# Performance work log

Hardware: AMD Instinct MI355X
Metric: run time of the kernel (lower is better)

Reference implementation:

```python
import jax, jax.numpy as jnp
import numpy as np

N = 4096        # nodes
D = 512         # in_dim = hidden_dim
E = 131072      # edges (avg degree 32)
K = 3           # aggregate_range
ALPHA = 2.0


def prelu(x, a):
    return jnp.where(x >= 0, x, a * x)


def setup_inputs() -> dict:
    key = jax.random.key(0)
    ks = jax.random.split(key, 8)
    s = 1.0 / np.sqrt(D)  # ~xavier scale
    return {
        "coeffs": jax.random.normal(ks[0], (N, D), jnp.float32),
        "edge_index": jax.random.randint(ks[1], (2, E), 0, N, dtype=jnp.int32),
        "W0": jax.random.normal(ks[2], (D, D), jnp.float32) * s,
        "b0": jnp.zeros((D,), jnp.float32),
        "a0": jnp.full((1,), 0.25, jnp.float32),
        "W1": jax.random.normal(ks[3], (D, D), jnp.float32) * s,  # use_bias=False
        "a1": jnp.full((1,), 0.25, jnp.float32),
        "W2": jax.random.normal(ks[4], (D, D), jnp.float32) * s,
        "a2": jnp.full((1,), 0.25, jnp.float32),
        "Wo": jax.random.normal(ks[5], (1, D), jnp.float32) * s,
        "bo": jnp.zeros((1,), jnp.float32),
    }


def _mlp(coeffs, W0, b0, a0, W1, a1, W2, a2, Wo, bo):
    # Linear+PReLU, then n_hidden_layers x [Linear(no bias)+PReLU+(Dropout: eval, no-op)], then Linear
    x = prelu(coeffs @ W0.T + b0, a0)
    x = prelu(x @ W1.T, a1)
    x = prelu(x @ W2.T, a2)
    return x @ Wo.T + bo  # [N, 1]


def _aggregate_k_hop(edge_index, angles):
    # Faithful to the torch code: enhanced_angles aliases angles, so each hop
    # reads the CURRENT (already enhanced) values:  a <- a + w_k * A_k @ a.
    # Hop 1 uses raw edge list (duplicate edges add twice). Hops >= 2 use
    # np.unique-deduplicated composed paths == boolean adjacency powers.
    src, dst = edge_index[0], edge_index[1]
    a = angles
    a = a + (0.5 ** ALPHA) * jax.ops.segment_sum(a[dst], src, num_segments=N)
    A = jnp.zeros((N, N), jnp.float32).at[src, dst].set(1.0)  # dedup'd boolean adjacency
    Ak = A
    for k_ in range(K - 1):
        Ak = ((Ak @ A) > 0).astype(jnp.float32)  # unique k-hop paths
        a = a + (1.0 / (k_ + 3)) ** ALPHA * (Ak @ a)
    return a


def reference(coeffs, edge_index, W0, b0, a0, W1, a1, W2, a2, Wo, bo):
    angles = _mlp(coeffs, W0, b0, a0, W1, a1, W2, a2, Wo, bo)
    return _aggregate_k_hop(edge_index, angles)
```

## Files before the change

### kernel.cpp

```cpp
#include <hip/hip_runtime.h>

#define N_NODES 4096
#define D_DIM   512
#define E_EDGES 131072
#define NWORDS  128

typedef __bf16 bf16;
typedef __bf16 bf16x4 __attribute__((ext_vector_type(4)));
typedef __bf16 bf16x8 __attribute__((ext_vector_type(8)));
typedef float  f32x4  __attribute__((ext_vector_type(4)));
typedef unsigned int u32;

#define GLOAD_LDS16(gp, lp) \
    __builtin_amdgcn_global_load_lds((const __attribute__((address_space(1))) u32*)(gp), \
                                     (__attribute__((address_space(3))) u32*)(lp), 16, 0, 0)

static const size_t OFF_W1B = 0;
static const size_t OFF_W2B = OFF_W1B + (size_t)D_DIM*D_DIM*2;
static const size_t OFF_X1  = OFF_W2B + (size_t)D_DIM*D_DIM*2;
static const size_t OFF_X2  = OFF_X1  + (size_t)N_NODES*D_DIM*2;
static const size_t OFF_ANG = OFF_X2  + (size_t)N_NODES*D_DIM*2;
static const size_t OFF_H1  = OFF_ANG + N_NODES*4;
static const size_t OFF_A2V = OFF_H1  + N_NODES*4;
static const size_t OFF_TP  = OFF_A2V + N_NODES*4;
static const size_t OFF_AB  = OFF_TP  + 1024*4;
static const size_t OFF_A2B = OFF_AB  + (size_t)N_NODES*NWORDS*4;
static const size_t OFF_A3B = OFF_A2B + (size_t)N_NODES*NWORDS*4;

__device__ __forceinline__ bf16x8 cvt8(float4 lo, float4 hi) {
    bf16x8 r;
    r[0] = (bf16)lo.x; r[1] = (bf16)lo.y; r[2] = (bf16)lo.z; r[3] = (bf16)lo.w;
    r[4] = (bf16)hi.x; r[5] = (bf16)hi.y; r[6] = (bf16)hi.z; r[7] = (bf16)hi.w;
    return r;
}

template<int MODE>
__global__ __launch_bounds__(256)
void gemm_fused(const float* __restrict__ Xf, const float* __restrict__ Wf,
                const bf16* __restrict__ X, const bf16* __restrict__ W,
                bf16* __restrict__ outB,
                const float* __restrict__ bias, const float* __restrict__ slope,
                const float* __restrict__ Wo, float* __restrict__ ang,
                const float* __restrict__ bo, float* __restrict__ h1,
                const float* __restrict__ W1f, const float* __restrict__ W2f,
                bf16* __restrict__ W1b, bf16* __restrict__ W2b,
                const int* __restrict__ esrc, const int* __restrict__ edst,
                u32* __restrict__ AbOut,
                const u32* __restrict__ P, const u32* __restrict__ Q, u32* __restrict__ BOut)
{
    __shared__ bf16 At[2][64][64];
    __shared__ bf16 Bt[2][64][64];
    __shared__ int  s_cnt[4];
    __shared__ int  s_list[4][256];
    const int bx = blockIdx.x;
    const int t = threadIdx.x;
    const int wave = t >> 6, lane = t & 63;

    if (bx < 512) {
        const int wm = wave >> 1, wn = wave & 1;
        const int quad = lane >> 4, lq = lane & 15;
        const int rowBase = (bx >> 3) * 64;
        const int colBase = (bx & 7) * 64;
        const int c0 = t, c1 = t + 256;
        const int r0 = c0 >> 3, o0 = (c0 & 7) * 8;
        const int r1 = c1 >> 3, o1 = (c1 & 7) * 8;

        f32x4 acc[2][2] = {};
        int cur = 0;

        if (MODE == 0) {
            const float* gA0 = Xf + (size_t)(rowBase + r0) * D_DIM + o0;
            const float* gA1 = Xf + (size_t)(rowBase + r1) * D_DIM + o1;
            const float* gB0 = Wf + (size_t)(colBase + r0) * D_DIM + o0;
            const float* gB1 = Wf + (size_t)(colBase + r1) * D_DIM + o1;
            float4 pa0l = *(const float4*)(gA0),     pa0h = *(const float4*)(gA0 + 4);
            float4 pa1l = *(const float4*)(gA1),     pa1h = *(const float4*)(gA1 + 4);
            float4 pb0l = *(const float4*)(gB0),     pb0h = *(const float4*)(gB0 + 4);
            float4 pb1l = *(const float4*)(gB1),     pb1h = *(const float4*)(gB1 + 4);
            for (int k0 = 0; k0 < D_DIM; k0 += 64) {
                *(bf16x8*)&At[cur][r0][o0] = cvt8(pa0l, pa0h);
                *(bf16x8*)&At[cur][r1][o1] = cvt8(pa1l, pa1h);
                *(bf16x8*)&Bt[cur][r0][o0] = cvt8(pb0l, pb0h);
                *(bf16x8*)&Bt[cur][r1][o1] = cvt8(pb1l, pb1h);
                if (k0 + 64 < D_DIM) {
                    pa0l = *(const float4*)(gA0 + k0 + 64); pa0h = *(const float4*)(gA0 + k0 + 68);
                    pa1l = *(const float4*)(gA1 + k0 + 64); pa1h = *(const float4*)(gA1 + k0 + 68);
                    pb0l = *(const float4*)(gB0 + k0 + 64); pb0h = *(const float4*)(gB0 + k0 + 68);
                    pb1l = *(const float4*)(gB1 + k0 + 64); pb1h = *(const float4*)(gB1 + k0 + 68);
                }
                __syncthreads();
                #pragma unroll
                for (int kc = 0; kc < 2; ++kc) {
                    bf16x8 af[2], bfr[2];
                    #pragma unroll
                    for (int tm = 0; tm < 2; ++tm) af[tm]  = *(const bf16x8*)&At[cur][wm * 32 + tm * 16 + lq][kc * 32 + quad * 8];
                    #pragma unroll
                    for (int tn = 0; tn < 2; ++tn) bfr[tn] = *(const bf16x8*)&Bt[cur][wn * 32 + tn * 16 + lq][kc * 32 + quad * 8];
                    #pragma unroll
                    for (int tm = 0; tm < 2; ++tm)
                        #pragma unroll
                        for (int tn = 0; tn < 2; ++tn)
                            acc[tm][tn] = __builtin_amdgcn_mfma_f32_16x16x32_bf16(af[tm], bfr[tn], acc[tm][tn], 0, 0, 0);
                }
                cur ^= 1;
            }
        } else {
            const bf16* gA0 = X + (size_t)(rowBase + r0) * D_DIM + o0;
            const bf16* gA1 = X + (size_t)(rowBase + r1) * D_DIM + o1;
            const bf16* gB0 = W + (size_t)(colBase + r0) * D_DIM + o0;
            const bf16* gB1 = W + (size_t)(colBase + r1) * D_DIM + o1;
            char* baseA = (char*)&At[0][0][0];
            char* baseB = (char*)&Bt[0][0][0];
            GLOAD_LDS16(gA0, baseA + wave * 1024);
            GLOAD_LDS16(gA1, baseA + 4096 + wave * 1024);
            GLOAD_LDS16(gB0, baseB + wave * 1024);
            GLOAD_LDS16(gB1, baseB + 4096 + wave * 1024);
            for (int k0 = 0; k0 < D_DIM; k0 += 64) {
                __syncthreads();
                if (k0 + 64 < D_DIM) {
                    int nb = (cur ^ 1) * 8192;
                    GLOAD_LDS16(gA0 + k0 + 64, baseA + nb + wave * 1024);
                    GLOAD_LDS16(gA1 + k0 + 64, baseA + nb + 4096 + wave * 1024);
                    GLOAD_LDS16(gB0 + k0 + 64, baseB + nb + wave * 1024);
                    GLOAD_LDS16(gB1 + k0 + 64, baseB + nb + 4096 + wave * 1024);
                }
                #pragma unroll
                for (int kc = 0; kc < 2; ++kc) {
                    bf16x8 af[2], bfr[2];
                    #pragma unroll
                    for (int tm = 0; tm < 2; ++tm) af[tm]  = *(const bf16x8*)&At[cur][wm * 32 + tm * 16 + lq][kc * 32 + quad * 8];
                    #pragma unroll
                    for (int tn = 0; tn < 2; ++tn) bfr[tn] = *(const bf16x8*)&Bt[cur][wn * 32 + tn * 16 + lq][kc * 32 + quad * 8];
                    #pragma unroll
                    for (int tm = 0; tm < 2; ++tm)
                        #pragma unroll
                        for (int tn = 0; tn < 2; ++tn)
                            acc[tm][tn] = __builtin_amdgcn_mfma_f32_16x16x32_bf16(af[tm], bfr[tn], acc[tm][tn], 0, 0, 0);
                }
                cur ^= 1;
            }
        }

        const float a = slope[0];
        if (MODE == 2) {
            float wo[2];
            #pragma unroll
            for (int tn = 0; tn < 2; ++tn) wo[tn] = Wo[colBase + wn * 32 + tn * 16 + lq];
            #pragma unroll
            for (int tm = 0; tm < 2; ++tm) {
                #pragma unroll
                for (int r = 0; r < 4; ++r) {
                    float p = 0.f;
                    #pragma unroll
                    for (int tn = 0; tn < 2; ++tn) {
                        float v = acc[tm][tn][r];
                        v = (v >= 0.f) ? v : a * v;
                        p += v * wo[tn];
                    }
                    #pragma unroll
                    for (int m = 1; m < 16; m <<= 1) p += __shfl_xor(p, m, 64);
                    if (lq == 0)
                        atomicAdd(&ang[rowBase + wm * 32 + tm * 16 + quad * 4 + r], p);
                }
            }
        } else {
            #pragma unroll
            for (int tm = 0; tm < 2; ++tm) {
                #pragma unroll
                for (int tn = 0; tn < 2; ++tn) {
                    int col = colBase + wn * 32 + tn * 16 + lq;
                    float b = (MODE == 0) ? bias[col] : 0.f;
                    #pragma unroll
                    for (int r = 0; r < 4; ++r) {
                        int row = rowBase + wm * 32 + tm * 16 + quad * 4 + r;
                        float v = acc[tm][tn][r] + b;
                        v = (v >= 0.f) ? v : a * v;
                        outB[(size_t)row * D_DIM + col] = (bf16)v;
                    }
                }
            }
        }
    } else if (MODE == 0) {
        if (bx < 640) {
            int base = (bx - 512) * 256 + t;
            for (int e = base; e < E_EDGES; e += 128 * 256) {
                int r = esrc[e], c = edst[e];
                atomicOr(&AbOut[(size_t)r * NWORDS + (c >> 5)], 1u << (c & 31));
            }
        } else if (bx < 768) {
            int cb = bx - 640;
            const float* src = (cb < 64) ? W1f : W2f;
            bf16* dst = (cb < 64) ? W1b : W2b;
            size_t base = (size_t)(cb & 63) * 4096;
            #pragma unroll
            for (int i = 0; i < 4; ++i) {
                size_t e = base + (size_t)(i * 256 + t) * 4;
                float4 v = *(const float4*)(src + e);
                bf16x4 o; o.x = (bf16)v.x; o.y = (bf16)v.y; o.z = (bf16)v.z; o.w = (bf16)v.w;
                *(bf16x4*)(dst + e) = o;
            }
        } else {
            float b = bo[0];
            for (int i = t; i < N_NODES; i += 256) { ang[i] = b; h1[i] = 0.f; }
        }
    } else {
        int row = (bx - 512) * 4 + wave;
        if (lane == 0) s_cnt[wave] = 0;
        __syncthreads();
        const u32* prow = P + (size_t)row * NWORDS;
        #pragma unroll
        for (int h = 0; h < 2; ++h) {
            u32 bits = prow[h * 64 + lane];
            int base = (h * 64 + lane) * 32;
            while (bits) {
                int b = __ffs(bits) - 1; bits &= bits - 1;
                int pos = atomicAdd(&s_cnt[wave], 1);
                if (pos < 256) s_list[wave][pos] = base + b;
            }
        }
        __syncthreads();
        int cnt = min(s_cnt[wave], 256);
        u32 acc0 = 0, acc1 = 0;
        int j = 0;
        for (; j + 4 <= cnt; j += 4) {
            int i0 = s_list[wave][j], i1 = s_list[wave][j + 1];
            int i2 = s_list[wave][j + 2], i3 = s_list[wave][j + 3];
            const u32* q0 = Q + (size_t)i0 * NWORDS;
            const u32* q1 = Q + (size_t)i1 * NWORDS;
            const u32* q2 = Q + (size_t)i2 * NWORDS;
            const u32* q3 = Q + (size_t)i3 * NWORDS;
            u32 x0 = q0[lane], x1 = q1[lane], x2 = q2[lane], x3 = q3[lane];
            u32 y0 = q0[64 + lane], y1 = q1[64 + lane], y2 = q2[64 + lane], y3 = q3[64 + lane];
            acc0 |= x0 | x1 | x2 | x3;
            acc1 |= y0 | y1 | y2 | y3;
        }
        for (; j < cnt; ++j) {
            const u32* q = Q + (size_t)s_list[wave][j] * NWORDS;
            acc0 |= q[lane]; acc1 |= q[64 + lane];
        }
        BOut[(size_t)row * NWORDS + lane]      = acc0;
        BOut[(size_t)row * NWORDS + 64 + lane] = acc1;
    }
}

__global__ __launch_bounds__(256)
void hop1_edges(const int* __restrict__ src, const int* __restrict__ dst,
                const float* __restrict__ ang, float* __restrict__ h1)
{
    int e = blockIdx.x * 256 + threadIdx.x;
    if (e < E_EDGES) atomicAdd(&h1[src[e]], 0.25f * ang[dst[e]]);
}

__global__ __launch_bounds__(256)
void bits_matvec2(const u32* __restrict__ A2, const float* __restrict__ ang,
                  const float* __restrict__ h1, float* __restrict__ a2,
                  float* __restrict__ Tpart)
{
    __shared__ float s_red[4];
    int wave = threadIdx.x >> 6, lane = threadIdx.x & 63;
    int row  = blockIdx.x * 4 + wave;
    float s = 0.f;
    #pragma unroll
    for (int h = 0; h < 2; ++h) {
        u32 bits = A2[(size_t)row * NWORDS + h * 64 + lane];
        int base = (h * 64 + lane) * 32;
        while (bits) {
            int b = __ffs(bits) - 1;
            bits &= bits - 1;
            s += ang[base + b] + h1[base + b];
        }
    }
    #pragma unroll
    for (int off = 32; off > 0; off >>= 1) s += __shfl_down(s, off, 64);
    if (lane == 0) {
        float val = (ang[row] + h1[row]) + (1.f / 9.f) * s;
        a2[row] = val;
        s_red[wave] = val;
    }
    __syncthreads();
    if (threadIdx.x == 0)
        Tpart[blockIdx.x] = s_red[0] + s_red[1] + s_red[2] + s_red[3];
}

__global__ __launch_bounds__(256)
void bits_matvec3(const u32* __restrict__ A3, const float* __restrict__ a2,
                  const float* __restrict__ Tpart, float* __restrict__ out)
{
    __shared__ float s_part[4];
    int wave = threadIdx.x >> 6, lane = threadIdx.x & 63;

    float tsum = 0.f;
    #pragma unroll
    for (int i = 0; i < 4; ++i) tsum += Tpart[i * 256 + threadIdx.x];
    #pragma unroll
    for (int off = 32; off > 0; off >>= 1) tsum += __shfl_down(tsum, off, 64);
    if (lane == 0) s_part[wave] = tsum;
    __syncthreads();
    const float T = s_part[0] + s_part[1] + s_part[2] + s_part[3];

    int row = blockIdx.x * 4 + wave;
    float s = 0.f;
    #pragma unroll
    for (int h = 0; h < 2; ++h) {
        u32 bits = ~A3[(size_t)row * NWORDS + h * 64 + lane];
        int base = (h * 64 + lane) * 32;
        while (bits) {
            int b = __ffs(bits) - 1;
            bits &= bits - 1;
            s += a2[base + b];
        }
    }
    #pragma unroll
    for (int off = 32; off > 0; off >>= 1) s += __shfl_down(s, off, 64);
    if (lane == 0) out[row] = a2[row] + (1.f / 16.f) * (T - s);
}

extern "C" void kernel_launch(void* const* d_in, const int* in_sizes, int n_in,
                              void* d_out, int out_size, void* d_ws, size_t ws_size,
                              hipStream_t stream) {
    const float* coeffs = (const float*)d_in[0];
    const int*   edges  = (const int*)d_in[1];
    const float* W0     = (const float*)d_in[2];
    const float* b0     = (const float*)d_in[3];
    const float* pa0    = (const float*)d_in[4];
    const float* W1     = (const float*)d_in[5];
    const float* pa1    = (const float*)d_in[6];
    const float* W2     = (const float*)d_in[7];
    const float* pa2    = (const float*)d_in[8];
    const float* Wo     = (const float*)d_in[9];
    const float* bo     = (const float*)d_in[10];
    float* out = (float*)d_out;

    char* ws = (char*)d_ws;
    bf16*  W1b  = (bf16*)(ws + OFF_W1B);
    bf16*  W2b  = (bf16*)(ws + OFF_W2B);
    bf16*  x1b  = (bf16*)(ws + OFF_X1);
    bf16*  x2b  = (bf16*)(ws + OFF_X2);
    float* ang  = (float*)(ws + OFF_ANG);
    float* h1   = (float*)(ws + OFF_H1);
    float* a2v  = (float*)(ws + OFF_A2V);
    float* Tp   = (float*)(ws + OFF_TP);
    u32*   Ab   = (u32*)(ws + OFF_AB);
    u32*   A2b  = (u32*)(ws + OFF_A2B);
    u32*   A3b  = (u32*)(ws + OFF_A3B);

    const int* srcp = edges;
    const int* dstp = edges + E_EDGES;

    hipMemsetAsync(Ab, 0, (size_t)N_NODES * NWORDS * 4, stream);

    gemm_fused<0><<<769, 256, 0, stream>>>(coeffs, W0, nullptr, nullptr, x1b, b0, pa0,
                                           nullptr, ang, bo, h1, W1, W2, W1b, W2b,
                                           srcp, dstp, Ab, nullptr, nullptr, nullptr);
    gemm_fused<1><<<1536, 256, 0, stream>>>(nullptr, nullptr, x1b, W1b, x2b, nullptr, pa1,
                                            nullptr, nullptr, nullptr, nullptr, nullptr, nullptr,
                                            nullptr, nullptr, nullptr, nullptr, nullptr, Ab, Ab, A2b);
    gemm_fused<2><<<1536, 256, 0, stream>>>(nullptr, nullptr, x2b, W2b, nullptr, nullptr, pa2,
                                            Wo, ang, nullptr, nullptr, nullptr, nullptr, nullptr, nullptr,
                                            nullptr, nullptr, nullptr, Ab, A2b, A3b);

    hop1_edges<<<E_EDGES / 256, 256, 0, stream>>>(srcp, dstp, ang, h1);
    bits_matvec2<<<N_NODES / 4, 256, 0, stream>>>(A2b, ang, h1, a2v, Tp);
    bits_matvec3<<<N_NODES / 4, 256, 0, stream>>>(A3b, a2v, Tp, out);
}
```

Measured before the change: 146.3 us.

## Fuse hop1, matvec2 and matvec3 into one persistent kernel with grid barriers

```diff
diff --git a/kernel.cpp b/kernel.cpp
--- a/kernel.cpp
+++ b/kernel.cpp
@@ -4,6 +4,7 @@
 #define D_DIM   512
 #define E_EDGES 131072
 #define NWORDS  128
+#define FIN_BLOCKS 512
 
 typedef __bf16 bf16;
 typedef __bf16 bf16x4 __attribute__((ext_vector_type(4)));
@@ -202,6 +203,7 @@
         } else {
             float b = bo[0];
             for (int i = t; i < N_NODES; i += 256) { ang[i] = b; h1[i] = 0.f; }
+            if (t < 4) BOut[t] = 0u;
         }
     } else {
         int row = (bx - 512) * 4 + wave;
@@ -244,75 +246,88 @@
 }
 
 __global__ __launch_bounds__(256)
-void hop1_edges(const int* __restrict__ src, const int* __restrict__ dst,
-                const float* __restrict__ ang, float* __restrict__ h1)
+void finalize(const int* __restrict__ src, const int* __restrict__ dst,
+              const float* __restrict__ ang, float* __restrict__ h1,
+              const u32* __restrict__ A2, float* __restrict__ a2,
+              const u32* __restrict__ A3, float* __restrict__ out,
+              int* __restrict__ bar, float* __restrict__ Tacc)
 {
-    int e = blockIdx.x * 256 + threadIdx.x;
-    if (e < E_EDGES) atomicAdd(&h1[src[e]], 0.25f * ang[dst[e]]);
-}
-
-__global__ __launch_bounds__(256)
-void bits_matvec2(const u32* __restrict__ A2, const float* __restrict__ ang,
-                  const float* __restrict__ h1, float* __restrict__ a2,
-                  float* __restrict__ Tpart)
-{
-    __shared__ float s_red[4];
-    int wave = threadIdx.x >> 6, lane = threadIdx.x & 63;
-    int row  = blockIdx.x * 4 + wave;
-    float s = 0.f;
+    __shared__ float s_red[8];
+    __shared__ float s_T;
+    const int t = threadIdx.x, wave = t >> 6, lane = t & 63;
+    const int bx = blockIdx.x;
+
+    {
+        int e = bx * 256 + t;
+        atomicAdd(&h1[src[e]], 0.25f * ang[dst[e]]);
+    }
+
+    __threadfence();
+    __syncthreads();
+    if (t == 0) {
+        __hip_atomic_fetch_add(bar, 1, __ATOMIC_ACQ_REL, __HIP_MEMORY_SCOPE_AGENT);
+        while (__hip_atomic_load(bar, __ATOMIC_ACQUIRE, __HIP_MEMORY_SCOPE_AGENT) < FIN_BLOCKS) {}
+    }
+    __syncthreads();
+    __threadfence();
+
     #pragma unroll
-    for (int h = 0; h < 2; ++h) {
-        u32 bits = A2[(size_t)row * NWORDS + h * 64 + lane];
-        int base = (h * 64 + lane) * 32;
-        while (bits) {
-            int b = __ffs(bits) - 1;
-            bits &= bits - 1;
-            s += ang[base + b] + h1[base + b];
-        }
-    }
+    for (int rr = 0; rr < 2; ++rr) {
+        int row = bx * 8 + wave * 2 + rr;
+        float s = 0.f;
+        #pragma unroll
+        for (int h = 0; h < 2; ++h) {
+            u32 bits = A2[(size_t)row * NWORDS + h * 64 + lane];
+            int base = (h * 64 + lane) * 32;
+            while (bits) {
+                int b = __ffs(bits) - 1; bits &= bits - 1;
+                s += ang[base + b] + h1[base + b];
+            }
+        }
+        #pragma unroll
+        for (int off = 32; off > 0; off >>= 1) s += __shfl_down(s, off, 64);
+        if (lane == 0) {
+            float val = (ang[row] + h1[row]) + (1.f / 9.f) * s;
+            a2[row] = val;
+            s_red[wave * 2 + rr] = val;
+        }
+    }
+    __syncthreads();
+    if (t == 0) {
+        float p = 0.f;
+        #pragma unroll
+        for (int i = 0; i < 8; ++i) p += s_red[i];
+        __hip_atomic_fetch_add(Tacc, p, __ATOMIC_RELAXED, __HIP_MEMORY_SCOPE_AGENT);
+    }
+
+    __threadfence();
+    __syncthreads();
+    if (t == 0) {
+        __hip_atomic_fetch_add(bar + 1, 1, __ATOMIC_ACQ_REL, __HIP_MEMORY_SCOPE_AGENT);
+        while (__hip_atomic_load(bar + 1, __ATOMIC_ACQUIRE, __HIP_MEMORY_SCOPE_AGENT) < FIN_BLOCKS) {}
+        s_T = __hip_atomic_load(Tacc, __ATOMIC_RELAXED, __HIP_MEMORY_SCOPE_AGENT);
+    }
+    __syncthreads();
+    __threadfence();
+    const float T = s_T;
+
     #pragma unroll
-    for (int off = 32; off > 0; off >>= 1) s += __shfl_down(s, off, 64);
-    if (lane == 0) {
-        float val = (ang[row] + h1[row]) + (1.f / 9.f) * s;
-        a2[row] = val;
-        s_red[wave] = val;
-    }
-    __syncthreads();
-    if (threadIdx.x == 0)
-        Tpart[blockIdx.x] = s_red[0] + s_red[1] + s_red[2] + s_red[3];
-}
-
-__global__ __launch_bounds__(256)
-void bits_matvec3(const u32* __restrict__ A3, const float* __restrict__ a2,
-                  const float* __restrict__ Tpart, float* __restrict__ out)
-{
-    __shared__ float s_part[4];
-    int wave = threadIdx.x >> 6, lane = threadIdx.x & 63;
-
-    float tsum = 0.f;
-    #pragma unroll
-    for (int i = 0; i < 4; ++i) tsum += Tpart[i * 256 + threadIdx.x];
-    #pragma unroll
-    for (int off = 32; off > 0; off >>= 1) tsum += __shfl_down(tsum, off, 64);
-    if (lane == 0) s_part[wave] = tsum;
-    __syncthreads();
-    const float T = s_part[0] + s_part[1] + s_part[2] + s_part[3];
-
-    int row = blockIdx.x * 4 + wave;
-    float s = 0.f;
-    #pragma unroll
-    for (int h = 0; h < 2; ++h) {
-        u32 bits = ~A3[(size_t)row * NWORDS + h * 64 + lane];
-        int base = (h * 64 + lane) * 32;
-        while (bits) {
-            int b = __ffs(bits) - 1;
-            bits &= bits - 1;
-            s += a2[base + b];
-        }
-    }
-    #pragma unroll
-    for (int off = 32; off > 0; off >>= 1) s += __shfl_down(s, off, 64);
-    if (lane == 0) out[row] = a2[row] + (1.f / 16.f) * (T - s);
+    for (int rr = 0; rr < 2; ++rr) {
+        int row = bx * 8 + wave * 2 + rr;
+        float s = 0.f;
+        #pragma unroll
+        for (int h = 0; h < 2; ++h) {
+            u32 bits = ~A3[(size_t)row * NWORDS + h * 64 + lane];
+            int base = (h * 64 + lane) * 32;
+            while (bits) {
+                int b = __ffs(bits) - 1; bits &= bits - 1;
+                s += a2[base + b];
+            }
+        }
+        #pragma unroll
+        for (int off = 32; off > 0; off >>= 1) s += __shfl_down(s, off, 64);
+        if (lane == 0) out[row] = a2[row] + (1.f / 16.f) * (T - s);
+    }
 }
 
 extern "C" void kernel_launch(void* const* d_in, const int* in_sizes, int n_in,
@@ -339,7 +354,7 @@
     float* ang  = (float*)(ws + OFF_ANG);
     float* h1   = (float*)(ws + OFF_H1);
     float* a2v  = (float*)(ws + OFF_A2V);
-    float* Tp   = (float*)(ws + OFF_TP);
+    u32*   ctl  = (u32*)(ws + OFF_TP);
     u32*   Ab   = (u32*)(ws + OFF_AB);
     u32*   A2b  = (u32*)(ws + OFF_A2B);
     u32*   A3b  = (u32*)(ws + OFF_A3B);
@@ -351,7 +366,7 @@
 
     gemm_fused<0><<<769, 256, 0, stream>>>(coeffs, W0, nullptr, nullptr, x1b, b0, pa0,
                                            nullptr, ang, bo, h1, W1, W2, W1b, W2b,
-                                           srcp, dstp, Ab, nullptr, nullptr, nullptr);
+                                           srcp, dstp, Ab, nullptr, nullptr, ctl);
     gemm_fused<1><<<1536, 256, 0, stream>>>(nullptr, nullptr, x1b, W1b, x2b, nullptr, pa1,
                                             nullptr, nullptr, nullptr, nullptr, nullptr, nullptr,
                                             nullptr, nullptr, nullptr, nullptr, nullptr, Ab, Ab, A2b);
@@ -359,7 +374,6 @@
                                             Wo, ang, nullptr, nullptr, nullptr, nullptr, nullptr, nullptr,
                                             nullptr, nullptr, nullptr, Ab, A2b, A3b);
 
-    hop1_edges<<<E_EDGES / 256, 256, 0, stream>>>(srcp, dstp, ang, h1);
-    bits_matvec2<<<N_NODES / 4, 256, 0, stream>>>(A2b, ang, h1, a2v, Tp);
-    bits_matvec3<<<N_NODES / 4, 256, 0, stream>>>(A3b, a2v, Tp, out);
+    finalize<<<FIN_BLOCKS, 256, 0, stream>>>(srcp, dstp, ang, h1, A2b, a2v, A3b, out,
+                                             (int*)ctl, (float*)(ctl + 2));
 }
```

Result: slower. 345.7 us (+136.3%).
